# Kernel optimization log

Hardware: AMD Instinct MI355X
Metric: run time of the kernel (lower is better)

Reference implementation:

```python
import jax, jax.numpy as jnp
import numpy as np

B, S, HID = 2, 2048, 2048
H, HKV = 16, 4
D = HID // H          # 128
N_REP = H // HKV      # 4
ROPE_THETA = 1000000.0


def _rope_tables(seq_len, head_dim, theta):
    inv_freq = 1.0 / (theta ** (jnp.arange(0, head_dim, 2, dtype=jnp.float32) / head_dim))
    freqs = jnp.arange(seq_len, dtype=jnp.float32)[:, None] * inv_freq[None, :]  # [S, D/2]
    emb = jnp.concatenate([freqs, freqs], axis=-1)  # [S, D]
    return jnp.cos(emb), jnp.sin(emb)


def setup_inputs() -> dict:
    key = jax.random.key(0)
    ks = jax.random.split(key, 6)
    cos, sin = _rope_tables(S, D, ROPE_THETA)
    sc = 0.02
    return {
        "x": jax.random.normal(ks[0], (B, S, HID), jnp.float32),
        "cos": cos,
        "sin": sin,
        "Wq": jax.random.normal(ks[1], (HID, H * D), jnp.float32) * sc,
        "Wk": jax.random.normal(ks[2], (HID, HKV * D), jnp.float32) * sc,
        "Wv": jax.random.normal(ks[3], (HID, HKV * D), jnp.float32) * sc,
        "Wo": jax.random.normal(ks[4], (H * D, HID), jnp.float32) * sc,
    }


def _rotate_half(t):
    t1, t2 = jnp.split(t, 2, axis=-1)
    return jnp.concatenate([-t2, t1], axis=-1)


def reference(x, cos, sin, Wq, Wk, Wv, Wo):
    b, s, _ = x.shape
    q = (x @ Wq).reshape(b, s, H, D)    # [b,s,H,d]
    k = (x @ Wk).reshape(b, s, HKV, D)  # [b,s,Hkv,d]
    v = (x @ Wv).reshape(b, s, HKV, D)

    # RoPE (cos/sin broadcast over head axis)
    c = cos[:s, None, :]  # [s,1,d]
    sn = sin[:s, None, :]
    q = q * c + _rotate_half(q) * sn
    k = k * c + _rotate_half(k) * sn

    # GQA: repeat kv heads (interleaved, matching repeat_kv)
    k = jnp.repeat(k, N_REP, axis=2)  # [b,s,H,d]
    v = jnp.repeat(v, N_REP, axis=2)

    q = q.transpose(0, 2, 1, 3)  # [b,H,s,d]
    k = k.transpose(0, 2, 1, 3)
    v = v.transpose(0, 2, 1, 3)

    scale = 1.0 / jnp.sqrt(jnp.asarray(D, x.dtype))
    scores = jnp.einsum("bhqd,bhkd->bhqk", q, k) * scale
    causal = jnp.tril(jnp.ones((s, s), dtype=bool))
    scores = jnp.where(causal[None, None], scores, jnp.asarray(-jnp.inf, scores.dtype))
    probs = jax.nn.softmax(scores, axis=-1)
    out = jnp.einsum("bhqk,bhkd->bhqd", probs, v)
    out = out.transpose(0, 2, 1, 3).reshape(b, s, H * D)
    return out @ Wo
```

## Files before the change

### kernel.cpp

```cpp
#include <hip/hip_runtime.h>
#include <cstdint>

#define B_    2
#define S_    2048
#define HID_  2048
#define H_    16
#define HKV_  4
#define D_    128
#define SCALE_ 0.08838834764831845f
#define LOG2E_ 1.4426950408889634f
#define K1_   (SCALE_ * LOG2E_)
#define THRS_ 62.75f

typedef __bf16 bf16x8 __attribute__((ext_vector_type(8)));
typedef float  f32x4  __attribute__((ext_vector_type(4)));
using u16 = unsigned short;

static __device__ __forceinline__ u16 f2bf(float f) {
  union { float f; uint32_t u; } c; c.f = f;
  uint32_t u = c.u;
  return (u16)((u + 0x7FFFu + ((u >> 16) & 1u)) >> 16);
}
static __device__ __forceinline__ float bf2f(u16 h) {
  union { uint32_t u; float f; } c; c.u = ((uint32_t)h) << 16;
  return c.f;
}
static __device__ __forceinline__ void async16(const u16* g, u16* lds) {
  __builtin_amdgcn_global_load_lds((const __attribute__((address_space(1))) void*)g,
                                   (__attribute__((address_space(3))) void*)lds, 16, 0, 0);
}

__global__ __launch_bounds__(256) void prep_cast_weights(const float* __restrict__ x,
                                                         const float* __restrict__ Wq,
                                                         const float* __restrict__ Wk,
                                                         const float* __restrict__ Wv,
                                                         const float* __restrict__ Wo,
                                                         u16* __restrict__ xb,
                                                         u16* __restrict__ Wt,
                                                         u16* __restrict__ Wot) {
  __shared__ float tile[32][33];
  const int t = blockIdx.x;
  const int tid = threadIdx.x;
  if (t < 8192) {
    const int i = t * 256 + tid;
    float4 v = ((const float4*)x)[i];
    ushort4 o;
    o.x = f2bf(v.x); o.y = f2bf(v.y); o.z = f2bf(v.z); o.w = f2bf(v.w);
    ((ushort4*)xb)[i] = o;
    return;
  }
  const int tw = t - 8192;
  const float* W; u16* Dst; int N, lt;
  if (tw < 4096)      { W = Wq; Dst = Wt;                        N = 2048; lt = tw; }
  else if (tw < 5120) { W = Wk; Dst = Wt + (size_t)2048 * 2048;  N = 512;  lt = tw - 4096; }
  else if (tw < 6144) { W = Wv; Dst = Wt + (size_t)2560 * 2048;  N = 512;  lt = tw - 5120; }
  else                { W = Wo; Dst = Wot;                       N = 2048; lt = tw - 6144; }
  const int tx = tid & 31, ty = tid >> 5;
  const int tn = N >> 5;
  const int n0 = (lt % tn) * 32, k0 = (lt / tn) * 32;
#pragma unroll
  for (int j = 0; j < 32; j += 8)
    tile[ty + j][tx] = W[(size_t)(k0 + ty + j) * N + n0 + tx];
  __syncthreads();
#pragma unroll
  for (int j = 0; j < 32; j += 8)
    Dst[(size_t)(n0 + ty + j) * 2048 + k0 + tx] = f2bf(tile[tx][ty + j]);
}

__global__ __launch_bounds__(256) void prep_rope_k(const u16* __restrict__ qkv,
                                                   const float* __restrict__ cosb,
                                                   const float* __restrict__ sinb,
                                                   u16* __restrict__ Kr) {
  const int idx = blockIdx.x * 256 + threadIdx.x;
  const int j = (idx & 31) * 2, rest = idx >> 5;
  const int kv = rest & 3, srow = rest >> 2;
  const int s = srow & (S_ - 1);
  const u16* base = qkv + (size_t)srow * 3072 + 2048 + kv * 128;
  const float2 cc = *(const float2*)&cosb[s * 128 + j];
  const float2 ss = *(const float2*)&sinb[s * 128 + j];
  const ushort2 av = *(const ushort2*)&base[j];
  const ushort2 bv = *(const ushort2*)&base[j + 64];
  const float a0 = bf2f(av.x), a1 = bf2f(av.y);
  const float b0 = bf2f(bv.x), b1 = bf2f(bv.y);
  const size_t ko = (((size_t)(srow >> 11) * HKV_ + kv) * S_ + s) * D_;
  ushort2 lo, hi;
  lo.x = f2bf(a0 * cc.x - b0 * ss.x); lo.y = f2bf(a1 * cc.y - b1 * ss.y);
  hi.x = f2bf(b0 * cc.x + a0 * ss.x); hi.y = f2bf(b1 * cc.y + a1 * ss.y);
  *(ushort2*)&Kr[ko + j]      = lo;
  *(ushort2*)&Kr[ko + j + 64] = hi;
}

template<int MODE>
__global__ __launch_bounds__(256, 3) void gemm_bt(const u16* __restrict__ A,
                                                  const u16* __restrict__ Bt,
                                                  void* __restrict__ Cv,
                                                  u16* __restrict__ Vt,
                                                  int M, int N, int K, int gx) {
  const int nwg = (int)gridDim.x;
  const int bid = (int)blockIdx.x;
  const int qq = nwg >> 3, rr = nwg & 7;
  const int xcd = bid & 7, pos = bid >> 3;
  const int wg = ((xcd < rr) ? xcd * (qq + 1) : rr * (qq + 1) + (xcd - rr) * qq) + pos;
  const int bm = (wg % gx) * 128;
  const int bn = (wg / gx) * 128;

  __shared__ __align__(16) u16 Ash[128 * 64];
  __shared__ __align__(16) u16 Bsh[128 * 64];
  const int tid = threadIdx.x;
  const int w = tid >> 6, l = tid & 63;
  const int wm = (w >> 1) * 64, wn = (w & 1) * 64;

  const f32x4 z4 = {0.f, 0.f, 0.f, 0.f};
  f32x4 acc[4][4];
#pragma unroll
  for (int i = 0; i < 4; ++i)
#pragma unroll
    for (int j = 0; j < 4; ++j) acc[i][j] = z4;

  const int srow = w * 8 + (l >> 3);
  const int schunk = l & 7;

  for (int k0 = 0; k0 < K; k0 += 64) {
#pragma unroll
    for (int i = 0; i < 4; ++i) {
      const int row = i * 32 + srow;
      const int ch = schunk ^ (row & 7);
      async16(A + (size_t)(bm + row) * K + k0 + ch * 8, &Ash[(i * 4 + w) * 512]);
      async16(Bt + (size_t)(bn + row) * K + k0 + ch * 8, &Bsh[(i * 4 + w) * 512]);
    }
    asm volatile("s_waitcnt vmcnt(0)" ::: "memory");
    __syncthreads();
#pragma unroll
    for (int kc = 0; kc < 2; ++kc) {
      bf16x8 af[4], bfr[4];
#pragma unroll
      for (int mi = 0; mi < 4; ++mi) {
        const int r = wm + mi * 16 + (l & 15);
        const int c2 = (kc * 4 + (l >> 4)) ^ (r & 7);
        af[mi] = *(const bf16x8*)&Ash[r * 64 + c2 * 8];
      }
#pragma unroll
      for (int ni = 0; ni < 4; ++ni) {
        const int r = wn + ni * 16 + (l & 15);
        const int c2 = (kc * 4 + (l >> 4)) ^ (r & 7);
        bfr[ni] = *(const bf16x8*)&Bsh[r * 64 + c2 * 8];
      }
#pragma unroll
      for (int mi = 0; mi < 4; ++mi)
#pragma unroll
        for (int ni = 0; ni < 4; ++ni)
          acc[mi][ni] = __builtin_amdgcn_mfma_f32_16x16x32_bf16(af[mi], bfr[ni], acc[mi][ni], 0, 0, 0);
    }
    __syncthreads();
  }

  if (MODE == 1 && bn >= 2560) {
    const int kv = (bn - 2560) >> 7;
#pragma unroll
    for (int mi = 0; mi < 4; ++mi) {
      const int r0 = bm + wm + mi * 16 + ((l >> 4) << 2);
      const int bb = r0 >> 11;
      const int s0 = r0 & (S_ - 1);
      const int a  = (s0 & 63) >> 2;
      const int pb = ((a >> 3) * 4 + (a & 3)) * 8 + ((a >> 2) & 1) * 4;
      const int spb = (s0 & ~63) | pb;
      u16* vb = Vt + ((size_t)(bb * HKV_ + kv) * D_) * S_ + spb;
#pragma unroll
      for (int ni = 0; ni < 4; ++ni) {
        const int d = wn + ni * 16 + (l & 15);
        ushort4 o;
        o.x = f2bf(acc[mi][ni][0]); o.y = f2bf(acc[mi][ni][1]);
        o.z = f2bf(acc[mi][ni][2]); o.w = f2bf(acc[mi][ni][3]);
        *(ushort4*)&vb[(size_t)d * S_] = o;
      }
    }
  } else {
#pragma unroll
    for (int mi = 0; mi < 4; ++mi) {
      const int r0 = bm + wm + mi * 16 + ((l >> 4) << 2);
#pragma unroll
      for (int ni = 0; ni < 4; ++ni) {
        const int c = bn + wn + ni * 16 + (l & 15);
#pragma unroll
        for (int j = 0; j < 4; ++j) {
          if (MODE == 1) ((u16*)Cv)[(size_t)(r0 + j) * N + c] = f2bf(acc[mi][ni][j]);
          else           ((float*)Cv)[(size_t)(r0 + j) * N + c] = acc[mi][ni][j];
        }
      }
    }
  }
}

__global__ __launch_bounds__(256, 3) void attn_kernel(const u16* __restrict__ qkv,
                                                      const float* __restrict__ cosb,
                                                      const float* __restrict__ sinb,
                                                      const u16* __restrict__ Kc,
                                                      const u16* __restrict__ Vt,
                                                      u16* __restrict__ O) {
  const int bid = blockIdx.x;
  const int p   = bid & 7;
  const int hs  = (bid >> 3) & 3;
  const int idx = bid >> 5;
  const int grp = idx >> 3, jj2 = idx & 7;
  const int qt  = (grp == 0) ? (31 - jj2) : (grp == 1) ? jj2
                : (grp == 2) ? (23 - jj2) : (8 + jj2);
  const int b   = p >> 2;
  const int kvh = p & 3;
  const int h   = kvh * 4 + hs;
  const int tid = threadIdx.x;
  const int w = tid >> 6, l = tid & 63;
  const int g = l >> 4, c = l & 15;
  const int q0 = qt * 64;

  __shared__ __align__(16) u16 Ksh[64 * 128];
  __shared__ __align__(16) u16 VshF[2 * 128 * 64];

  const u16* Kbase = Kc + ((size_t)(b * HKV_ + kvh) * S_) * D_;
  const u16* Vbase = Vt + ((size_t)(b * HKV_ + kvh) * D_) * S_;

  bf16x8 qf[4];
  {
    const u16* Qb = qkv + ((size_t)b * S_ + q0) * 3072 + h * 128;
#pragma unroll
    for (int i = 0; i < 4; ++i) {
      const int rQ = i * 16 + w * 4 + g;
      async16(Qb + (size_t)rQ * 3072 + (c ^ (rQ & 7)) * 8, &VshF[i * 2048 + w * 512]);
    }
    asm volatile("s_waitcnt vmcnt(0)" ::: "memory");
    __builtin_amdgcn_sched_barrier(0);
    __builtin_amdgcn_s_barrier();
    const int rr = w * 16 + c;
    const int s_q = q0 + rr;
    bf16x8 qraw[4];
#pragma unroll
    for (int kc = 0; kc < 4; ++kc)
      qraw[kc] = *(const bf16x8*)&VshF[rr * 128 + ((kc * 4 + g) ^ (c & 7)) * 8];
    const float* cp = cosb + s_q * 128 + g * 8;
    const float* sp = sinb + s_q * 128 + g * 8;
#pragma unroll
    for (int kcp = 0; kcp < 2; ++kcp) {
      float cl[8], sl[8];
      *(float4*)&cl[0] = *(const float4*)(cp + kcp * 32);
      *(float4*)&cl[4] = *(const float4*)(cp + kcp * 32 + 4);
      *(float4*)&sl[0] = *(const float4*)(sp + kcp * 32);
      *(float4*)&sl[4] = *(const float4*)(sp + kcp * 32 + 4);
      bf16x8 lo, hi;
#pragma unroll
      for (int j = 0; j < 8; ++j) {
        const float a  = (float)qraw[kcp][j];
        const float b2 = (float)qraw[kcp + 2][j];
        lo[j] = (__bf16)(a * cl[j] - b2 * sl[j]);
        hi[j] = (__bf16)(b2 * cl[j] + a * sl[j]);
      }
      qf[kcp] = lo; qf[kcp + 2] = hi;
    }
    asm volatile("s_waitcnt lgkmcnt(0)" ::: "memory");
    __builtin_amdgcn_sched_barrier(0);
    __builtin_amdgcn_s_barrier();
  }

  int srcK[4], srcV[4];
#pragma unroll
  for (int i = 0; i < 4; ++i) {
    const int rK = i * 16 + w * 4 + g;
    srcK[i] = rK * 128 + (c ^ (rK & 7)) * 8;
    const int dV = i * 32 + w * 8 + (l >> 3);
    srcV[i] = dV * S_ + ((l & 7) ^ (dV & 7)) * 8;
  }

  const f32x4 z4 = {0.f, 0.f, 0.f, 0.f};
  f32x4 oacc[8];
#pragma unroll
  for (int nb = 0; nb < 8; ++nb) oacc[nb] = z4;
  float m_i = -1e30f, l_i = 0.f;

  auto stageK = [&](int kv0) {
#pragma unroll
    for (int i = 0; i < 4; ++i)
      async16(Kbase + (size_t)kv0 * 128 + srcK[i], &Ksh[i * 2048 + w * 512]);
  };
  auto stageV = [&](int buf, int kv0) {
#pragma unroll
    for (int i = 0; i < 4; ++i)
      async16(Vbase + kv0 + srcV[i], &VshF[buf * 8192 + i * 2048 + w * 512]);
  };

  const int nt = qt + 1;
  stageV(0, 0);
  stageK(0);

  for (int t = 0; t < nt; ++t) {
    const int cur = t & 1;
    asm volatile("s_waitcnt vmcnt(0) lgkmcnt(0)" ::: "memory");
    __builtin_amdgcn_sched_barrier(0);
    __builtin_amdgcn_s_barrier();
    if (t + 1 < nt) stageV(cur ^ 1, (t + 1) << 6);

    f32x4 sf[4];
#pragma unroll
    for (int nb = 0; nb < 4; ++nb) sf[nb] = z4;

    __builtin_amdgcn_s_setprio(1);
#pragma unroll
    for (int kc = 0; kc < 4; ++kc) {
#pragma unroll
      for (int nb = 0; nb < 4; ++nb) {
        const int r = nb * 16 + c;
        const int s2 = (kc * 4 + g) ^ (c & 7);
        const bf16x8 kf = *(const bf16x8*)&Ksh[r * 128 + s2 * 8];
        sf[nb] = __builtin_amdgcn_mfma_f32_16x16x32_bf16(kf, qf[kc], sf[nb], 0, 0, 0);
      }
    }
    __builtin_amdgcn_s_setprio(0);

    asm volatile("s_waitcnt lgkmcnt(0)" ::: "memory");
    __builtin_amdgcn_sched_barrier(0);
    __builtin_amdgcn_s_barrier();
    if (t + 1 < nt) stageK((t + 1) << 6);

    {
      const int kv0 = t << 6;
      const int qcol = q0 + w * 16 + c;
      const bool doMask = (t == nt - 1);
      float mx = -3e38f;
#pragma unroll
      for (int nb = 0; nb < 4; ++nb)
#pragma unroll
        for (int jj = 0; jj < 4; ++jj) {
          float sv = sf[nb][jj];
          if (doMask) {
            const int kk = kv0 + nb * 16 + g * 4 + jj;
            sv = (kk > qcol) ? -3e38f : sv;
            sf[nb][jj] = sv;
          }
          mx = fmaxf(mx, sv);
        }
      mx = fmaxf(mx, __shfl_xor(mx, 16));
      mx = fmaxf(mx, __shfl_xor(mx, 32));

      if (__all(mx <= m_i + THRS_)) {
        const float mk = m_i * K1_;
        float rs = 0.f;
#pragma unroll
        for (int nb = 0; nb < 4; ++nb)
#pragma unroll
          for (int jj = 0; jj < 4; ++jj) {
            const float p2 = exp2f(fmaf(sf[nb][jj], K1_, -mk));
            sf[nb][jj] = p2;
            rs += p2;
          }
        rs += __shfl_xor(rs, 16);
        rs += __shfl_xor(rs, 32);
        l_i += rs;
      } else {
        const float mnew = fmaxf(m_i, mx);
        const float fsc = exp2f((m_i - mnew) * K1_);
        m_i = mnew;
        const float mk = mnew * K1_;
        float rs = 0.f;
#pragma unroll
        for (int nb = 0; nb < 4; ++nb)
#pragma unroll
          for (int jj = 0; jj < 4; ++jj) {
            const float p2 = exp2f(fmaf(sf[nb][jj], K1_, -mk));
            sf[nb][jj] = p2;
            rs += p2;
          }
        rs += __shfl_xor(rs, 16);
        rs += __shfl_xor(rs, 32);
        l_i = l_i * fsc + rs;
        float fq[4];
#pragma unroll
        for (int j = 0; j < 4; ++j) fq[j] = __shfl(fsc, g * 4 + j);
#pragma unroll
        for (int nb = 0; nb < 8; ++nb)
#pragma unroll
          for (int j = 0; j < 4; ++j) oacc[nb][j] *= fq[j];
      }
    }

    bf16x8 pa, pb;
#pragma unroll
    for (int jj = 0; jj < 4; ++jj) {
      pa[jj] = (__bf16)sf[0][jj]; pa[4 + jj] = (__bf16)sf[1][jj];
      pb[jj] = (__bf16)sf[2][jj]; pb[4 + jj] = (__bf16)sf[3][jj];
    }

    const char* Vb = (const char*)&VshF[cur * 8192] + c * 128;
    __builtin_amdgcn_s_setprio(1);
#pragma unroll
    for (int kc2 = 0; kc2 < 2; ++kc2) {
      const bf16x8 pfr = kc2 ? pb : pa;
      const int s2v = ((kc2 * 4 + g) ^ (c & 7)) << 4;
#pragma unroll
      for (int nb = 0; nb < 8; ++nb) {
        const bf16x8 vf = *(const bf16x8*)(Vb + nb * 2048 + s2v);
        oacc[nb] = __builtin_amdgcn_mfma_f32_16x16x32_bf16(pfr, vf, oacc[nb], 0, 0, 0);
      }
    }
    __builtin_amdgcn_s_setprio(0);
  }

#pragma unroll
  for (int j = 0; j < 4; ++j) {
    const float li = __shfl(l_i, g * 4 + j);
    const float inv = 1.f / li;
    const int srow = q0 + w * 16 + g * 4 + j;
    u16* op = O + ((size_t)(b * S_ + srow)) * HID_ + h * D_ + c;
#pragma unroll
    for (int nb = 0; nb < 8; ++nb) op[nb * 16] = f2bf(oacc[nb][j] * inv);
  }
}

extern "C" void kernel_launch(void* const* d_in, const int* in_sizes, int n_in,
                              void* d_out, int out_size, void* d_ws, size_t ws_size,
                              hipStream_t stream) {
  const float* x    = (const float*)d_in[0];
  const float* cosb = (const float*)d_in[1];
  const float* sinb = (const float*)d_in[2];
  const float* Wq   = (const float*)d_in[3];
  const float* Wk   = (const float*)d_in[4];
  const float* Wv   = (const float*)d_in[5];
  const float* Wo   = (const float*)d_in[6];
  float* out = (float*)d_out;

  u16*   xb   = (u16*)d_ws;
  u16*   Wt   = xb  + (size_t)4096 * 2048;
  u16*   Wot  = Wt  + (size_t)3072 * 2048;
  u16*   qkv  = Wot + (size_t)2048 * 2048;
  u16*   Kr   = qkv + (size_t)4096 * 3072;
  u16*   Vtb  = Kr  + (size_t)B_ * HKV_ * S_ * D_;
  u16*   Ob   = Vtb + (size_t)B_ * HKV_ * S_ * D_;

  prep_cast_weights<<<dim3(18432), 256, 0, stream>>>(x, Wq, Wk, Wv, Wo, xb, Wt, Wot);

  gemm_bt<1><<<dim3(768), 256, 0, stream>>>(xb, Wt, qkv, Vtb, 4096, 3072, 2048, 32);

  prep_rope_k<<<dim3(2048), 256, 0, stream>>>(qkv, cosb, sinb, Kr);

  attn_kernel<<<dim3(1024), 256, 0, stream>>>(qkv, cosb, sinb, Kr, Vtb, Ob);

  gemm_bt<0><<<dim3(512), 256, 0, stream>>>(Ob, Wot, out, nullptr, 4096, 2048, 2048, 32);
}
```

Before: 197.1 us.

## Double attention query tile to 128 rows with 8 waves sharing K/V tiles

The attention kernel now uses 512-thread blocks covering 128 query rows, so each K/V tile staged in shared memory serves twice as many queries and the grid halves to 512 blocks. Staging loops are rewritten for the larger thread count, and waves whose rows lie entirely above the causal diagonal skip compute on the final tiles. The query-tile scheduling order is simplified to a two-group reverse/forward pattern. The larger blocks reduce shared-memory traffic per query, at the cost of fewer blocks, coarser load balance across CUs, and idle waves on diagonal tiles.

```diff
diff --git a/kernel.cpp b/kernel.cpp
--- a/kernel.cpp
+++ b/kernel.cpp
@@ -191,7 +191,7 @@
   }
 }
 
-__global__ __launch_bounds__(256, 3) void attn_kernel(const u16* __restrict__ qkv,
+__global__ __launch_bounds__(512, 2) void attn_kernel(const u16* __restrict__ qkv,
                                                       const float* __restrict__ cosb,
                                                       const float* __restrict__ sinb,
                                                       const u16* __restrict__ Kc,
@@ -200,32 +200,53 @@
   const int bid = blockIdx.x;
   const int p   = bid & 7;
   const int hs  = (bid >> 3) & 3;
-  const int idx = bid >> 5;
-  const int grp = idx >> 3, jj2 = idx & 7;
-  const int qt  = (grp == 0) ? (31 - jj2) : (grp == 1) ? jj2
-                : (grp == 2) ? (23 - jj2) : (8 + jj2);
+  const int qtidx = bid >> 5;
+  const int qt  = (bid < 256) ? (15 - qtidx) : (qtidx - 8);
   const int b   = p >> 2;
   const int kvh = p & 3;
   const int h   = kvh * 4 + hs;
   const int tid = threadIdx.x;
   const int w = tid >> 6, l = tid & 63;
   const int g = l >> 4, c = l & 15;
-  const int q0 = qt * 64;
+  const int q0 = qt * 128;
 
   __shared__ __align__(16) u16 Ksh[64 * 128];
-  __shared__ __align__(16) u16 VshF[2 * 128 * 64];
+  __shared__ __align__(16) u16 VshF[2 * 64 * 128];
 
   const u16* Kbase = Kc + ((size_t)(b * HKV_ + kvh) * S_) * D_;
   const u16* Vbase = Vt + ((size_t)(b * HKV_ + kvh) * D_) * S_;
+
+  auto stageK = [&](int kv0) {
+#pragma unroll
+    for (int i = 0; i < 2; ++i) {
+      const int o = i * 512 + tid;
+      const int rK = o >> 4;
+      const int gr = o & 15;
+      async16(Kbase + (size_t)(kv0 + rK) * 128 + (gr ^ (rK & 7)) * 8, &Ksh[o * 8]);
+    }
+  };
+  auto stageV = [&](int buf, int kv0) {
+#pragma unroll
+    for (int i = 0; i < 2; ++i) {
+      const int o = i * 512 + tid;
+      const int dV = o >> 3;
+      const int sl = o & 7;
+      async16(Vbase + (size_t)dV * S_ + kv0 + ((sl ^ (dV & 7)) * 8),
+              &VshF[buf * 8192 + o * 8]);
+    }
+  };
 
   bf16x8 qf[4];
   {
     const u16* Qb = qkv + ((size_t)b * S_ + q0) * 3072 + h * 128;
 #pragma unroll
     for (int i = 0; i < 4; ++i) {
-      const int rQ = i * 16 + w * 4 + g;
-      async16(Qb + (size_t)rQ * 3072 + (c ^ (rQ & 7)) * 8, &VshF[i * 2048 + w * 512]);
-    }
+      const int o = i * 512 + tid;
+      const int rQ = o >> 4;
+      const int gr = o & 15;
+      async16(Qb + (size_t)rQ * 3072 + (gr ^ (rQ & 7)) * 8, &VshF[o * 8]);
+    }
+    stageK(0);
     asm volatile("s_waitcnt vmcnt(0)" ::: "memory");
     __builtin_amdgcn_sched_barrier(0);
     __builtin_amdgcn_s_barrier();
@@ -259,146 +280,128 @@
     __builtin_amdgcn_s_barrier();
   }
 
-  int srcK[4], srcV[4];
-#pragma unroll
-  for (int i = 0; i < 4; ++i) {
-    const int rK = i * 16 + w * 4 + g;
-    srcK[i] = rK * 128 + (c ^ (rK & 7)) * 8;
-    const int dV = i * 32 + w * 8 + (l >> 3);
-    srcV[i] = dV * S_ + ((l & 7) ^ (dV & 7)) * 8;
-  }
-
   const f32x4 z4 = {0.f, 0.f, 0.f, 0.f};
   f32x4 oacc[8];
 #pragma unroll
   for (int nb = 0; nb < 8; ++nb) oacc[nb] = z4;
   float m_i = -1e30f, l_i = 0.f;
 
-  auto stageK = [&](int kv0) {
-#pragma unroll
-    for (int i = 0; i < 4; ++i)
-      async16(Kbase + (size_t)kv0 * 128 + srcK[i], &Ksh[i * 2048 + w * 512]);
-  };
-  auto stageV = [&](int buf, int kv0) {
-#pragma unroll
-    for (int i = 0; i < 4; ++i)
-      async16(Vbase + kv0 + srcV[i], &VshF[buf * 8192 + i * 2048 + w * 512]);
-  };
-
-  const int nt = qt + 1;
+  const int nt = 2 * (qt + 1);
   stageV(0, 0);
-  stageK(0);
 
   for (int t = 0; t < nt; ++t) {
     const int cur = t & 1;
-    asm volatile("s_waitcnt vmcnt(0) lgkmcnt(0)" ::: "memory");
-    __builtin_amdgcn_sched_barrier(0);
-    __builtin_amdgcn_s_barrier();
+    const int kv0 = t << 6;
+    asm volatile("s_waitcnt vmcnt(0)" ::: "memory");
+    __syncthreads();
     if (t + 1 < nt) stageV(cur ^ 1, (t + 1) << 6);
 
+    const bool live = (kv0 <= q0 + w * 16 + 15);
+
     f32x4 sf[4];
 #pragma unroll
     for (int nb = 0; nb < 4; ++nb) sf[nb] = z4;
 
-    __builtin_amdgcn_s_setprio(1);
-#pragma unroll
-    for (int kc = 0; kc < 4; ++kc) {
-#pragma unroll
-      for (int nb = 0; nb < 4; ++nb) {
-        const int r = nb * 16 + c;
-        const int s2 = (kc * 4 + g) ^ (c & 7);
-        const bf16x8 kf = *(const bf16x8*)&Ksh[r * 128 + s2 * 8];
-        sf[nb] = __builtin_amdgcn_mfma_f32_16x16x32_bf16(kf, qf[kc], sf[nb], 0, 0, 0);
-      }
-    }
-    __builtin_amdgcn_s_setprio(0);
-
-    asm volatile("s_waitcnt lgkmcnt(0)" ::: "memory");
-    __builtin_amdgcn_sched_barrier(0);
-    __builtin_amdgcn_s_barrier();
+    if (live) {
+      __builtin_amdgcn_s_setprio(1);
+#pragma unroll
+      for (int kc = 0; kc < 4; ++kc) {
+#pragma unroll
+        for (int nb = 0; nb < 4; ++nb) {
+          const int r = nb * 16 + c;
+          const int s2 = (kc * 4 + g) ^ (c & 7);
+          const bf16x8 kf = *(const bf16x8*)&Ksh[r * 128 + s2 * 8];
+          sf[nb] = __builtin_amdgcn_mfma_f32_16x16x32_bf16(kf, qf[kc], sf[nb], 0, 0, 0);
+        }
+      }
+      __builtin_amdgcn_s_setprio(0);
+    }
+
+    __syncthreads();
     if (t + 1 < nt) stageK((t + 1) << 6);
 
-    {
-      const int kv0 = t << 6;
-      const int qcol = q0 + w * 16 + c;
-      const bool doMask = (t == nt - 1);
-      float mx = -3e38f;
-#pragma unroll
-      for (int nb = 0; nb < 4; ++nb)
-#pragma unroll
-        for (int jj = 0; jj < 4; ++jj) {
-          float sv = sf[nb][jj];
-          if (doMask) {
-            const int kk = kv0 + nb * 16 + g * 4 + jj;
-            sv = (kk > qcol) ? -3e38f : sv;
-            sf[nb][jj] = sv;
+    if (live) {
+      {
+        const int qcol = q0 + w * 16 + c;
+        const bool doMask = (kv0 + 63 > q0 + w * 16);
+        float mx = -3e38f;
+#pragma unroll
+        for (int nb = 0; nb < 4; ++nb)
+#pragma unroll
+          for (int jj = 0; jj < 4; ++jj) {
+            float sv = sf[nb][jj];
+            if (doMask) {
+              const int kk = kv0 + nb * 16 + g * 4 + jj;
+              sv = (kk > qcol) ? -3e38f : sv;
+              sf[nb][jj] = sv;
+            }
+            mx = fmaxf(mx, sv);
           }
-          mx = fmaxf(mx, sv);
+        mx = fmaxf(mx, __shfl_xor(mx, 16));
+        mx = fmaxf(mx, __shfl_xor(mx, 32));
+
+        if (__all(mx <= m_i + THRS_)) {
+          const float mk = m_i * K1_;
+          float rs = 0.f;
+#pragma unroll
+          for (int nb = 0; nb < 4; ++nb)
+#pragma unroll
+            for (int jj = 0; jj < 4; ++jj) {
+              const float p2 = exp2f(fmaf(sf[nb][jj], K1_, -mk));
+              sf[nb][jj] = p2;
+              rs += p2;
+            }
+          rs += __shfl_xor(rs, 16);
+          rs += __shfl_xor(rs, 32);
+          l_i += rs;
+        } else {
+          const float mnew = fmaxf(m_i, mx);
+          const float fsc = exp2f((m_i - mnew) * K1_);
+          m_i = mnew;
+          const float mk = mnew * K1_;
+          float rs = 0.f;
+#pragma unroll
+          for (int nb = 0; nb < 4; ++nb)
+#pragma unroll
+            for (int jj = 0; jj < 4; ++jj) {
+              const float p2 = exp2f(fmaf(sf[nb][jj], K1_, -mk));
+              sf[nb][jj] = p2;
+              rs += p2;
+            }
+          rs += __shfl_xor(rs, 16);
+          rs += __shfl_xor(rs, 32);
+          l_i = l_i * fsc + rs;
+          float fq[4];
+#pragma unroll
+          for (int j = 0; j < 4; ++j) fq[j] = __shfl(fsc, g * 4 + j);
+#pragma unroll
+          for (int nb = 0; nb < 8; ++nb)
+#pragma unroll
+            for (int j = 0; j < 4; ++j) oacc[nb][j] *= fq[j];
         }
-      mx = fmaxf(mx, __shfl_xor(mx, 16));
-      mx = fmaxf(mx, __shfl_xor(mx, 32));
-
-      if (__all(mx <= m_i + THRS_)) {
-        const float mk = m_i * K1_;
-        float rs = 0.f;
-#pragma unroll
-        for (int nb = 0; nb < 4; ++nb)
-#pragma unroll
-          for (int jj = 0; jj < 4; ++jj) {
-            const float p2 = exp2f(fmaf(sf[nb][jj], K1_, -mk));
-            sf[nb][jj] = p2;
-            rs += p2;
-          }
-        rs += __shfl_xor(rs, 16);
-        rs += __shfl_xor(rs, 32);
-        l_i += rs;
-      } else {
-        const float mnew = fmaxf(m_i, mx);
-        const float fsc = exp2f((m_i - mnew) * K1_);
-        m_i = mnew;
-        const float mk = mnew * K1_;
-        float rs = 0.f;
-#pragma unroll
-        for (int nb = 0; nb < 4; ++nb)
-#pragma unroll
-          for (int jj = 0; jj < 4; ++jj) {
-            const float p2 = exp2f(fmaf(sf[nb][jj], K1_, -mk));
-            sf[nb][jj] = p2;
-            rs += p2;
-          }
-        rs += __shfl_xor(rs, 16);
-        rs += __shfl_xor(rs, 32);
-        l_i = l_i * fsc + rs;
-        float fq[4];
-#pragma unroll
-        for (int j = 0; j < 4; ++j) fq[j] = __shfl(fsc, g * 4 + j);
-#pragma unroll
-        for (int nb = 0; nb < 8; ++nb)
-#pragma unroll
-          for (int j = 0; j < 4; ++j) oacc[nb][j] *= fq[j];
-      }
-    }
-
-    bf16x8 pa, pb;
-#pragma unroll
-    for (int jj = 0; jj < 4; ++jj) {
-      pa[jj] = (__bf16)sf[0][jj]; pa[4 + jj] = (__bf16)sf[1][jj];
-      pb[jj] = (__bf16)sf[2][jj]; pb[4 + jj] = (__bf16)sf[3][jj];
-    }
-
-    const char* Vb = (const char*)&VshF[cur * 8192] + c * 128;
-    __builtin_amdgcn_s_setprio(1);
-#pragma unroll
-    for (int kc2 = 0; kc2 < 2; ++kc2) {
-      const bf16x8 pfr = kc2 ? pb : pa;
-      const int s2v = ((kc2 * 4 + g) ^ (c & 7)) << 4;
-#pragma unroll
-      for (int nb = 0; nb < 8; ++nb) {
-        const bf16x8 vf = *(const bf16x8*)(Vb + nb * 2048 + s2v);
-        oacc[nb] = __builtin_amdgcn_mfma_f32_16x16x32_bf16(pfr, vf, oacc[nb], 0, 0, 0);
-      }
-    }
-    __builtin_amdgcn_s_setprio(0);
+      }
+
+      bf16x8 pa, pb;
+#pragma unroll
+      for (int jj = 0; jj < 4; ++jj) {
+        pa[jj] = (__bf16)sf[0][jj]; pa[4 + jj] = (__bf16)sf[1][jj];
+        pb[jj] = (__bf16)sf[2][jj]; pb[4 + jj] = (__bf16)sf[3][jj];
+      }
+
+      const char* Vb = (const char*)&VshF[cur * 8192] + c * 128;
+      __builtin_amdgcn_s_setprio(1);
+#pragma unroll
+      for (int kc2 = 0; kc2 < 2; ++kc2) {
+        const bf16x8 pfr = kc2 ? pb : pa;
+        const int s2v = ((kc2 * 4 + g) ^ (c & 7)) << 4;
+#pragma unroll
+        for (int nb = 0; nb < 8; ++nb) {
+          const bf16x8 vf = *(const bf16x8*)(Vb + nb * 2048 + s2v);
+          oacc[nb] = __builtin_amdgcn_mfma_f32_16x16x32_bf16(pfr, vf, oacc[nb], 0, 0, 0);
+        }
+      }
+      __builtin_amdgcn_s_setprio(0);
+    }
   }
 
 #pragma unroll
@@ -438,7 +441,7 @@
 
   prep_rope_k<<<dim3(2048), 256, 0, stream>>>(qkv, cosb, sinb, Kr);
 
-  attn_kernel<<<dim3(1024), 256, 0, stream>>>(qkv, cosb, sinb, Kr, Vtb, Ob);
+  attn_kernel<<<dim3(512), 512, 0, stream>>>(qkv, cosb, sinb, Kr, Vtb, Ob);
 
   gemm_bt<0><<<dim3(512), 256, 0, stream>>>(Ob, Wot, out, nullptr, 4096, 2048, 2048, 32);
 }
```

Result: slower. 226.1 us (+14.7%).
